# Optimization experiments

Measured on AMD Instinct MI355X. Metric: run time of the kernel, lower is better.

The kernel has to match this reference:

```python
import jax, jax.numpy as jnp
import numpy as np

N = 65536
E = 1048576
DIN = 64
DOUT = 64


def setup_inputs() -> dict:
    key = jax.random.key(0)
    ks = jax.random.split(key, 16)
    inp = {
        'feat': jax.random.normal(ks[0], (N, DIN), dtype=jnp.float32),
        'norm': jax.random.uniform(ks[1], (N, 1), dtype=jnp.float32),
        'src': jax.random.randint(ks[2], (E,), 0, N, dtype=jnp.int32),
        'dst': jax.random.randint(ks[3], (E,), 0, N, dtype=jnp.int32),
    }
    s = 0.05
    inp['W_self'] = jax.random.normal(ks[4], (DOUT, DIN)) * s
    inp['b_self'] = jnp.zeros((DOUT,), jnp.float32)
    inp['W_self_high'] = jax.random.normal(ks[5], (DOUT, DIN)) * s
    inp['b_self_high'] = jnp.zeros((DOUT,), jnp.float32)
    inp['W_neigh'] = jax.random.normal(ks[6], (DOUT, DIN)) * s
    inp['b_neigh'] = jnp.zeros((DOUT,), jnp.float32)
    inp['W_neigh_high'] = jax.random.normal(ks[7], (DOUT, DIN)) * s
    inp['b_neigh_high'] = jnp.zeros((DOUT,), jnp.float32)
    inp['W_id'] = jax.random.normal(ks[8], (DOUT, DIN)) * s
    inp['b_id'] = jnp.zeros((DOUT,), jnp.float32)
    inp['w_att_low'] = jax.random.normal(ks[9], (1, DOUT)) * s
    inp['w_att_high'] = jax.random.normal(ks[10], (1, DOUT)) * s
    inp['w_att_mlp'] = jax.random.normal(ks[11], (1, DOUT)) * s
    inp['W_att'] = jax.random.normal(ks[12], (3, 3)) * s
    return inp


def _linear(x, W, b):
    return x @ W.T + b


def _mean_agg(h, norm, src, dst, n_nodes):
    # copy_src('h','m') of (h * norm), then mean-reduce by dst node
    msg = (h * norm)[src]                                   # [E, D] gather
    summed = jax.ops.segment_sum(msg, dst, num_segments=n_nodes)
    deg = jax.ops.segment_sum(jnp.ones((dst.shape[0],), h.dtype), dst,
                              num_segments=n_nodes)
    return summed / jnp.maximum(deg, 1.0)[:, None]          # zero-in-degree -> 0


def reference(feat, norm, src, dst,
              W_self, b_self, W_self_high, b_self_high,
              W_neigh, b_neigh, W_neigh_high, b_neigh_high,
              W_id, b_id, w_att_low, w_att_high, w_att_mlp, W_att):
    n = feat.shape[0]
    # variant=True branch of acmgraphsage
    self_low = jax.nn.relu(_linear(feat, W_self, b_self))
    self_high = jax.nn.relu(_linear(feat, W_self_high, b_self_high))
    neigh_low = _mean_agg(jax.nn.relu(_linear(feat, W_neigh, b_neigh)),
                          norm, src, dst, n)
    neigh_high = _mean_agg(jax.nn.relu(_linear(feat, W_neigh_high, b_neigh_high)),
                           norm, src, dst, n)
    low = self_low + neigh_low
    high = self_high - neigh_high
    identity = jax.nn.relu(_linear(feat, W_id, b_id))
    # attention: sigmoid of per-branch scalar logits -> 3x3 mix -> softmax/T
    logits = jnp.concatenate([low @ w_att_low.T,
                              high @ w_att_high.T,
                              identity @ w_att_mlp.T], axis=1)   # [N, 3]
    att = jax.nn.softmax((jax.nn.sigmoid(logits) @ W_att.T) / 3.0, axis=1)
    rst = 3.0 * (att[:, 0:1] * low + att[:, 1:2] * high + att[:, 2:3] * identity)
    return rst
```

## Files before the change

### kernel.cpp

```cpp
#include <hip/hip_runtime.h>
#include <stdint.h>


#define NBLK 256
#define NBUC 1024
#define NPB  64
#define GCAP 2048
#define MTOT (NBUC * NBLK)

__device__ __forceinline__ void load_feat(const float* __restrict__ feat, size_t base,
                                          float* __restrict__ f) {
    const float4* fp = (const float4*)(feat + base);
#pragma unroll
    for (int i = 0; i < 16; ++i) {
        float4 v = fp[i];
        f[4 * i + 0] = v.x; f[4 * i + 1] = v.y;
        f[4 * i + 2] = v.z; f[4 * i + 3] = v.w;
    }
}

__device__ __forceinline__ uint32_t bf16_rne(float x) {
    uint32_t u = __float_as_uint(x);
    return (u + 0x7fffu + ((u >> 16) & 1u)) >> 16;
}

__global__ void __launch_bounds__(512)
k_transform(const float* __restrict__ feat, const float* __restrict__ norm,
            const float* __restrict__ Wn, const float* __restrict__ bn,
            const float* __restrict__ Wnh, const float* __restrict__ bnh,
            uint32_t* __restrict__ h_pk, int N)
{
    int t = threadIdx.x;
    int nsub = t & 63;
    int q = __builtin_amdgcn_readfirstlane(t >> 6);
    int n = blockIdx.x * 64 + nsub;
    if (n >= N) return;

    size_t base = (size_t)n << 6;
    float f[64];
    load_feat(feat, base, f);
    float nr = norm[n];

    uint32_t pk[8];
#pragma unroll
    for (int jj = 0; jj < 8; ++jj) {
        int j = q * 8 + jj;
        const float4* rL = (const float4*)(Wn  + ((size_t)j << 6));
        const float4* rH = (const float4*)(Wnh + ((size_t)j << 6));
        float sL = 0.f, sH = 0.f;
#pragma unroll
        for (int k4 = 0; k4 < 16; ++k4) {
            float4 wL = rL[k4];
            float4 wH = rH[k4];
            sL = fmaf(f[4*k4+0], wL.x, sL); sL = fmaf(f[4*k4+1], wL.y, sL);
            sL = fmaf(f[4*k4+2], wL.z, sL); sL = fmaf(f[4*k4+3], wL.w, sL);
            sH = fmaf(f[4*k4+0], wH.x, sH); sH = fmaf(f[4*k4+1], wH.y, sH);
            sH = fmaf(f[4*k4+2], wH.z, sH); sH = fmaf(f[4*k4+3], wH.w, sH);
        }
        float oL = fmaxf(sL + bn[j],  0.f) * nr;
        float oH = fmaxf(sH + bnh[j], 0.f) * nr;
        pk[jj] = bf16_rne(oL) | (bf16_rne(oH) << 16);
    }
    uint4* pp = (uint4*)(h_pk + base + q * 8);
    pp[0] = make_uint4(pk[0], pk[1], pk[2], pk[3]);
    pp[1] = make_uint4(pk[4], pk[5], pk[6], pk[7]);
}

__global__ void __launch_bounds__(512)
k_bin_hist(const int* __restrict__ dst, int* __restrict__ blk_cnt, int E)
{
    __shared__ int cnt[NBUC];
    int t = threadIdx.x;
    for (int i = t; i < NBUC; i += 512) cnt[i] = 0;
    __syncthreads();
    int epb = (E + NBLK - 1) / NBLK;
    int eb = blockIdx.x * epb;
    for (int i0 = t * 8; i0 < epb; i0 += 512 * 8) {
        int e = eb + i0;
        if (e + 8 <= E) {
            int4 d0 = *(const int4*)(dst + e);
            int4 d1 = *(const int4*)(dst + e + 4);
            atomicAdd(&cnt[((unsigned)d0.x) >> 6], 1);
            atomicAdd(&cnt[((unsigned)d0.y) >> 6], 1);
            atomicAdd(&cnt[((unsigned)d0.z) >> 6], 1);
            atomicAdd(&cnt[((unsigned)d0.w) >> 6], 1);
            atomicAdd(&cnt[((unsigned)d1.x) >> 6], 1);
            atomicAdd(&cnt[((unsigned)d1.y) >> 6], 1);
            atomicAdd(&cnt[((unsigned)d1.z) >> 6], 1);
            atomicAdd(&cnt[((unsigned)d1.w) >> 6], 1);
        } else {
            for (int j = 0; j < 8; ++j) {
                int ee = e + j;
                if (ee < E) atomicAdd(&cnt[((unsigned)dst[ee]) >> 6], 1);
            }
        }
    }
    __syncthreads();
    for (int i = t; i < NBUC; i += 512)
        blk_cnt[i * NBLK + blockIdx.x] = cnt[i];
}

__global__ void __launch_bounds__(256)
k_scan_part(const int* __restrict__ cnt_in, int* __restrict__ part)
{
    __shared__ int red[256];
    int t = threadIdx.x;
    const int4* A4 = (const int4*)cnt_in;
    int4 v = A4[blockIdx.x * 256 + t];
    int s = v.x + v.y + v.z + v.w;
    red[t] = s;
    __syncthreads();
    for (int off = 128; off > 0; off >>= 1) {
        if (t < off) red[t] += red[t + off];
        __syncthreads();
    }
    if (t == 0) part[blockIdx.x] = red[0];
}

__global__ void __launch_bounds__(256)
k_scan_top(const int* __restrict__ part, int* __restrict__ top)
{
    __shared__ int s[256];
    int t = threadIdx.x;
    int mine = part[t];
    s[t] = mine;
    __syncthreads();
    for (int off = 1; off < 256; off <<= 1) {
        int v = s[t];
        int a = (t >= off) ? s[t - off] : 0;
        __syncthreads();
        s[t] = v + a;
        __syncthreads();
    }
    top[t] = s[t] - mine;
}

__global__ void __launch_bounds__(256)
k_scan_down(const int* __restrict__ cnt_in, const int* __restrict__ top,
            int* __restrict__ off_out)
{
    __shared__ int s[256];
    int t = threadIdx.x;
    const int4* A4 = (const int4*)cnt_in;
    int4 v = A4[blockIdx.x * 256 + t];
    int sum = v.x + v.y + v.z + v.w;
    s[t] = sum;
    __syncthreads();
    for (int off = 1; off < 256; off <<= 1) {
        int vv = s[t];
        int a = (t >= off) ? s[t - off] : 0;
        __syncthreads();
        s[t] = vv + a;
        __syncthreads();
    }
    int run = top[blockIdx.x] + s[t] - sum;
    int4 o;
    o.x = run; run += v.x;
    o.y = run; run += v.y;
    o.z = run; run += v.z;
    o.w = run; run += v.w;
    ((int4*)off_out)[blockIdx.x * 256 + t] = o;
    if (blockIdx.x == 255 && t == 255) off_out[MTOT] = run;
}

__global__ void __launch_bounds__(512)
k_bin_scatter(const int* __restrict__ src, const int* __restrict__ dst,
              const int* __restrict__ blk_off, uint32_t* __restrict__ ebuf, int E)
{
    __shared__ int base_[NBUC];
    __shared__ int cnt[NBUC];
    int t = threadIdx.x;
    for (int i = t; i < NBUC; i += 512) {
        base_[i] = blk_off[i * NBLK + blockIdx.x];
        cnt[i] = 0;
    }
    __syncthreads();
    int epb = (E + NBLK - 1) / NBLK;
    int eb = blockIdx.x * epb;
    for (int i0 = t * 8; i0 < epb; i0 += 512 * 8) {
        int e = eb + i0;
        if (e + 8 <= E) {
            int4 d0 = *(const int4*)(dst + e);
            int4 d1 = *(const int4*)(dst + e + 4);
            int4 s0 = *(const int4*)(src + e);
            int4 s1 = *(const int4*)(src + e + 4);
            int da[8] = { d0.x, d0.y, d0.z, d0.w, d1.x, d1.y, d1.z, d1.w };
            int sa[8] = { s0.x, s0.y, s0.z, s0.w, s1.x, s1.y, s1.z, s1.w };
#pragma unroll
            for (int j = 0; j < 8; ++j) {
                int b = ((unsigned)da[j]) >> 6;
                int r = atomicAdd(&cnt[b], 1);
                ebuf[base_[b] + r] = ((uint32_t)(da[j] & 63) << 16) | (uint32_t)sa[j];
            }
        } else {
            for (int j = 0; j < 8; ++j) {
                int ee = e + j;
                if (ee < E) {
                    int d = dst[ee];
                    int b = ((unsigned)d) >> 6;
                    int r = atomicAdd(&cnt[b], 1);
                    ebuf[base_[b] + r] = ((uint32_t)(d & 63) << 16) | (uint32_t)src[ee];
                }
            }
        }
    }
}

__global__ void __launch_bounds__(512)
k_gf(const uint32_t* __restrict__ h_pk, const int* __restrict__ blk_off,
     const uint32_t* __restrict__ ebuf,
     const float* __restrict__ feat,
     const float* __restrict__ Ws, const float* __restrict__ bs,
     const float* __restrict__ Wsh, const float* __restrict__ bsh,
     const float* __restrict__ Wid, const float* __restrict__ bid,
     const float* __restrict__ wl, const float* __restrict__ wh,
     const float* __restrict__ wm, const float* __restrict__ Watt,
     float* __restrict__ out, int N)
{
    __shared__ unsigned short sorted[GCAP];
    __shared__ int s_cnt[NPB];
    __shared__ int s_off[NPB];
    __shared__ float s_mL[NPB][65];
    __shared__ float s_mH[NPB][65];
    __shared__ float red[3][8][64];

    int b = blockIdx.x;
    int t = threadIdx.x;
    int es = blk_off[b * NBLK];
    int ee = blk_off[(b + 1) * NBLK];
    int ne = ee - es;
    if (ne > GCAP) ne = GCAP;
    if (t < NPB) s_cnt[t] = 0;
    __syncthreads();

    int ed[4], er[4], esrc[4];
#pragma unroll
    for (int i = 0; i < 4; ++i) {
        int idx = i * 512 + t;
        ed[i] = -1;
        if (idx < ne) {
            uint32_t v = ebuf[es + idx];
            ed[i] = (int)(v >> 16);
            esrc[i] = (int)(v & 0xffffu);
            er[i] = atomicAdd(&s_cnt[ed[i]], 1);
        }
    }
    __syncthreads();
    if (t < 64) {
        int c = s_cnt[t];
        int sc = c;
        for (int o = 1; o < 64; o <<= 1) {
            int u = __shfl_up(sc, o, 64);
            if (t >= o) sc += u;
        }
        s_off[t] = sc - c;
    }
    __syncthreads();
#pragma unroll
    for (int i = 0; i < 4; ++i)
        if (ed[i] >= 0) sorted[s_off[ed[i]] + er[i]] = (unsigned short)esrc[i];
    __syncthreads();

    int w = t >> 6, lane = t & 63;
    for (int dd = 0; dd < 8; ++dd) {
        int d = w * 8 + dd;
        int cd = s_cnt[d];
        int od = s_off[d];
        float accL = 0.f, accH = 0.f;
        int i = 0;
        for (; i + 4 <= cd; i += 4) {
            int s0 = sorted[od + i + 0];
            int s1 = sorted[od + i + 1];
            int s2 = sorted[od + i + 2];
            int s3 = sorted[od + i + 3];
            uint32_t v0 = h_pk[((size_t)s0 << 6) + lane];
            uint32_t v1 = h_pk[((size_t)s1 << 6) + lane];
            uint32_t v2 = h_pk[((size_t)s2 << 6) + lane];
            uint32_t v3 = h_pk[((size_t)s3 << 6) + lane];
            accL += __uint_as_float(v0 << 16) + __uint_as_float(v1 << 16)
                  + __uint_as_float(v2 << 16) + __uint_as_float(v3 << 16);
            accH += __uint_as_float(v0 & 0xffff0000u) + __uint_as_float(v1 & 0xffff0000u)
                  + __uint_as_float(v2 & 0xffff0000u) + __uint_as_float(v3 & 0xffff0000u);
        }
        for (; i < cd; ++i) {
            int s0 = sorted[od + i];
            uint32_t v0 = h_pk[((size_t)s0 << 6) + lane];
            accL += __uint_as_float(v0 << 16);
            accH += __uint_as_float(v0 & 0xffff0000u);
        }
        float inv = 1.f / fmaxf((float)cd, 1.f);
        s_mL[d][lane] = accL * inv;
        s_mH[d][lane] = accH * inv;
    }
    __syncthreads();

    int nsub = t & 63;
    int q = __builtin_amdgcn_readfirstlane(t >> 6);
    int n = b * 64 + nsub;
    size_t base = (size_t)n << 6;

    float f[64];
    load_feat(feat, base, f);

    float aL[8], aH[8], aI[8];
    float dLp = 0.f, dHp = 0.f, dIp = 0.f;
#pragma unroll
    for (int jj = 0; jj < 8; ++jj) {
        int j = q * 8 + jj;
        const float4* rL = (const float4*)(Ws  + ((size_t)j << 6));
        const float4* rH = (const float4*)(Wsh + ((size_t)j << 6));
        const float4* rI = (const float4*)(Wid + ((size_t)j << 6));
        float sL = 0.f, sH = 0.f, sI = 0.f;
#pragma unroll
        for (int k4 = 0; k4 < 16; ++k4) {
            float4 wL = rL[k4];
            float4 wH = rH[k4];
            float4 wI = rI[k4];
            sL = fmaf(f[4*k4+0], wL.x, sL); sL = fmaf(f[4*k4+1], wL.y, sL);
            sL = fmaf(f[4*k4+2], wL.z, sL); sL = fmaf(f[4*k4+3], wL.w, sL);
            sH = fmaf(f[4*k4+0], wH.x, sH); sH = fmaf(f[4*k4+1], wH.y, sH);
            sH = fmaf(f[4*k4+2], wH.z, sH); sH = fmaf(f[4*k4+3], wH.w, sH);
            sI = fmaf(f[4*k4+0], wI.x, sI); sI = fmaf(f[4*k4+1], wI.y, sI);
            sI = fmaf(f[4*k4+2], wI.z, sI); sI = fmaf(f[4*k4+3], wI.w, sI);
        }
        float lowj  = fmaxf(sL + bs[j],  0.f) + s_mL[nsub][j];
        float highj = fmaxf(sH + bsh[j], 0.f) - s_mH[nsub][j];
        float idj   = fmaxf(sI + bid[j], 0.f);
        aL[jj] = lowj; aH[jj] = highj; aI[jj] = idj;
        dLp = fmaf(lowj,  wl[j], dLp);
        dHp = fmaf(highj, wh[j], dHp);
        dIp = fmaf(idj,   wm[j], dIp);
    }

    red[0][q][nsub] = dLp;
    red[1][q][nsub] = dHp;
    red[2][q][nsub] = dIp;
    __syncthreads();
    float dL = 0.f, dH = 0.f, dI = 0.f;
#pragma unroll
    for (int p = 0; p < 8; ++p) {
        dL += red[0][p][nsub];
        dH += red[1][p][nsub];
        dI += red[2][p][nsub];
    }

    float s0 = 1.f / (1.f + expf(-dL));
    float s1 = 1.f / (1.f + expf(-dH));
    float s2 = 1.f / (1.f + expf(-dI));
    const float third = (1.f / 3.f);
    float z0 = (Watt[0] * s0 + Watt[1] * s1 + Watt[2] * s2) * third;
    float z1 = (Watt[3] * s0 + Watt[4] * s1 + Watt[5] * s2) * third;
    float z2 = (Watt[6] * s0 + Watt[7] * s1 + Watt[8] * s2) * third;
    float m = fmaxf(z0, fmaxf(z1, z2));
    float e0 = expf(z0 - m), e1 = expf(z1 - m), e2 = expf(z2 - m);
    float r = 3.f / (e0 + e1 + e2);
    float a0 = e0 * r, a1 = e1 * r, a2 = e2 * r;

    float o[8];
#pragma unroll
    for (int jj = 0; jj < 8; ++jj)
        o[jj] = a0 * aL[jj] + a1 * aH[jj] + a2 * aI[jj];
    float* po = out + base + q * 8;
    *(float4*)(po + 0) = make_float4(o[0], o[1], o[2], o[3]);
    *(float4*)(po + 4) = make_float4(o[4], o[5], o[6], o[7]);
}

extern "C" void kernel_launch(void* const* d_in, const int* in_sizes, int n_in,
                              void* d_out, int out_size, void* d_ws, size_t ws_size,
                              hipStream_t stream) {
    const float* feat         = (const float*)d_in[0];
    const float* norm         = (const float*)d_in[1];
    const int*   src          = (const int*)d_in[2];
    const int*   dst          = (const int*)d_in[3];
    const float* W_self       = (const float*)d_in[4];
    const float* b_self       = (const float*)d_in[5];
    const float* W_self_high  = (const float*)d_in[6];
    const float* b_self_high  = (const float*)d_in[7];
    const float* W_neigh      = (const float*)d_in[8];
    const float* b_neigh      = (const float*)d_in[9];
    const float* W_neigh_high = (const float*)d_in[10];
    const float* b_neigh_high = (const float*)d_in[11];
    const float* W_id         = (const float*)d_in[12];
    const float* b_id         = (const float*)d_in[13];
    const float* w_att_low    = (const float*)d_in[14];
    const float* w_att_high   = (const float*)d_in[15];
    const float* w_att_mlp    = (const float*)d_in[16];
    const float* W_att        = (const float*)d_in[17];

    int N = in_sizes[0] / 64;
    int E = in_sizes[2];
    float* out = (float*)d_out;

    size_t N64 = (size_t)N * 64;

    uint32_t* h_pk    = (uint32_t*)d_ws;
    int*      blk_cnt = (int*)(h_pk + N64);
    int*      blk_off = blk_cnt + MTOT;
    int*      part    = blk_off + MTOT + 16;
    int*      top     = part + 256 + 16;
    uint32_t* ebuf    = (uint32_t*)(top + 256 + 16);

    dim3 gN64((N + 63) / 64);

    k_transform<<<gN64, dim3(512), 0, stream>>>(feat, norm, W_neigh, b_neigh,
                                                W_neigh_high, b_neigh_high,
                                                h_pk, N);
    k_bin_hist<<<dim3(NBLK), dim3(512), 0, stream>>>(dst, blk_cnt, E);
    k_scan_part<<<dim3(256), dim3(256), 0, stream>>>(blk_cnt, part);
    k_scan_top<<<dim3(1), dim3(256), 0, stream>>>(part, top);
    k_scan_down<<<dim3(256), dim3(256), 0, stream>>>(blk_cnt, top, blk_off);
    k_bin_scatter<<<dim3(NBLK), dim3(512), 0, stream>>>(src, dst, blk_off, ebuf, E);
    k_gf<<<dim3(NBUC), dim3(512), 0, stream>>>(h_pk, blk_off, ebuf, feat,
                                               W_self, b_self,
                                               W_self_high, b_self_high,
                                               W_id, b_id, w_att_low, w_att_high,
                                               w_att_mlp, W_att, out, N);
}
```

Measured before the change: 138.7 us.

## Fuse transform and histogram kernels, unroll gather by eight, pack mean in bf16

Merges the neighbour-transform kernel and the destination histogram kernel into one launch, where extra blocks do the histogram, so the two independent stages can overlap and one launch is saved. The gather loop gets an 8-wide unrolled path with pairwise summation, putting more independent loads in flight per warp. The per-node mean for the low and high branches is packed into one bf16x2 shared array, which halves that LDS footprint but adds another rounding of the aggregated values. The fused kernel now carries the 4 KB histogram shared array in every block, which may reduce occupancy for the transform blocks.

```diff
diff --git a/kernel.cpp b/kernel.cpp
--- a/kernel.cpp
+++ b/kernel.cpp
@@ -25,12 +25,48 @@
 }
 
 __global__ void __launch_bounds__(512)
-k_transform(const float* __restrict__ feat, const float* __restrict__ norm,
-            const float* __restrict__ Wn, const float* __restrict__ bn,
-            const float* __restrict__ Wnh, const float* __restrict__ bnh,
-            uint32_t* __restrict__ h_pk, int N)
-{
-    int t = threadIdx.x;
+k_tf_hist(const float* __restrict__ feat, const float* __restrict__ norm,
+          const float* __restrict__ Wn, const float* __restrict__ bn,
+          const float* __restrict__ Wnh, const float* __restrict__ bnh,
+          uint32_t* __restrict__ h_pk,
+          const int* __restrict__ dst, int* __restrict__ blk_cnt,
+          int N, int E, int nTf)
+{
+    __shared__ int cnt[NBUC];
+    int t = threadIdx.x;
+
+    if ((int)blockIdx.x >= nTf) {
+        int hb = blockIdx.x - nTf;
+        for (int i = t; i < NBUC; i += 512) cnt[i] = 0;
+        __syncthreads();
+        int epb = (E + NBLK - 1) / NBLK;
+        int eb = hb * epb;
+        for (int i0 = t * 8; i0 < epb; i0 += 512 * 8) {
+            int e = eb + i0;
+            if (e + 8 <= E) {
+                int4 d0 = *(const int4*)(dst + e);
+                int4 d1 = *(const int4*)(dst + e + 4);
+                atomicAdd(&cnt[((unsigned)d0.x) >> 6], 1);
+                atomicAdd(&cnt[((unsigned)d0.y) >> 6], 1);
+                atomicAdd(&cnt[((unsigned)d0.z) >> 6], 1);
+                atomicAdd(&cnt[((unsigned)d0.w) >> 6], 1);
+                atomicAdd(&cnt[((unsigned)d1.x) >> 6], 1);
+                atomicAdd(&cnt[((unsigned)d1.y) >> 6], 1);
+                atomicAdd(&cnt[((unsigned)d1.z) >> 6], 1);
+                atomicAdd(&cnt[((unsigned)d1.w) >> 6], 1);
+            } else {
+                for (int j = 0; j < 8; ++j) {
+                    int ee = e + j;
+                    if (ee < E) atomicAdd(&cnt[((unsigned)dst[ee]) >> 6], 1);
+                }
+            }
+        }
+        __syncthreads();
+        for (int i = t; i < NBUC; i += 512)
+            blk_cnt[i * NBLK + hb] = cnt[i];
+        return;
+    }
+
     int nsub = t & 63;
     int q = __builtin_amdgcn_readfirstlane(t >> 6);
     int n = blockIdx.x * 64 + nsub;
@@ -64,40 +100,6 @@
     uint4* pp = (uint4*)(h_pk + base + q * 8);
     pp[0] = make_uint4(pk[0], pk[1], pk[2], pk[3]);
     pp[1] = make_uint4(pk[4], pk[5], pk[6], pk[7]);
-}
-
-__global__ void __launch_bounds__(512)
-k_bin_hist(const int* __restrict__ dst, int* __restrict__ blk_cnt, int E)
-{
-    __shared__ int cnt[NBUC];
-    int t = threadIdx.x;
-    for (int i = t; i < NBUC; i += 512) cnt[i] = 0;
-    __syncthreads();
-    int epb = (E + NBLK - 1) / NBLK;
-    int eb = blockIdx.x * epb;
-    for (int i0 = t * 8; i0 < epb; i0 += 512 * 8) {
-        int e = eb + i0;
-        if (e + 8 <= E) {
-            int4 d0 = *(const int4*)(dst + e);
-            int4 d1 = *(const int4*)(dst + e + 4);
-            atomicAdd(&cnt[((unsigned)d0.x) >> 6], 1);
-            atomicAdd(&cnt[((unsigned)d0.y) >> 6], 1);
-            atomicAdd(&cnt[((unsigned)d0.z) >> 6], 1);
-            atomicAdd(&cnt[((unsigned)d0.w) >> 6], 1);
-            atomicAdd(&cnt[((unsigned)d1.x) >> 6], 1);
-            atomicAdd(&cnt[((unsigned)d1.y) >> 6], 1);
-            atomicAdd(&cnt[((unsigned)d1.z) >> 6], 1);
-            atomicAdd(&cnt[((unsigned)d1.w) >> 6], 1);
-        } else {
-            for (int j = 0; j < 8; ++j) {
-                int ee = e + j;
-                if (ee < E) atomicAdd(&cnt[((unsigned)dst[ee]) >> 6], 1);
-            }
-        }
-    }
-    __syncthreads();
-    for (int i = t; i < NBUC; i += 512)
-        blk_cnt[i * NBLK + blockIdx.x] = cnt[i];
 }
 
 __global__ void __launch_bounds__(256)
@@ -220,8 +222,7 @@
     __shared__ unsigned short sorted[GCAP];
     __shared__ int s_cnt[NPB];
     __shared__ int s_off[NPB];
-    __shared__ float s_mL[NPB][65];
-    __shared__ float s_mH[NPB][65];
+    __shared__ uint32_t s_m[NPB][65];
     __shared__ float red[3][8][64];
 
     int b = blockIdx.x;
@@ -268,6 +269,32 @@
         int od = s_off[d];
         float accL = 0.f, accH = 0.f;
         int i = 0;
+        for (; i + 8 <= cd; i += 8) {
+            int s0 = sorted[od + i + 0];
+            int s1 = sorted[od + i + 1];
+            int s2 = sorted[od + i + 2];
+            int s3 = sorted[od + i + 3];
+            int s4 = sorted[od + i + 4];
+            int s5 = sorted[od + i + 5];
+            int s6 = sorted[od + i + 6];
+            int s7 = sorted[od + i + 7];
+            uint32_t v0 = h_pk[((size_t)s0 << 6) + lane];
+            uint32_t v1 = h_pk[((size_t)s1 << 6) + lane];
+            uint32_t v2 = h_pk[((size_t)s2 << 6) + lane];
+            uint32_t v3 = h_pk[((size_t)s3 << 6) + lane];
+            uint32_t v4 = h_pk[((size_t)s4 << 6) + lane];
+            uint32_t v5 = h_pk[((size_t)s5 << 6) + lane];
+            uint32_t v6 = h_pk[((size_t)s6 << 6) + lane];
+            uint32_t v7 = h_pk[((size_t)s7 << 6) + lane];
+            accL += (__uint_as_float(v0 << 16) + __uint_as_float(v1 << 16))
+                  + (__uint_as_float(v2 << 16) + __uint_as_float(v3 << 16))
+                  + (__uint_as_float(v4 << 16) + __uint_as_float(v5 << 16))
+                  + (__uint_as_float(v6 << 16) + __uint_as_float(v7 << 16));
+            accH += (__uint_as_float(v0 & 0xffff0000u) + __uint_as_float(v1 & 0xffff0000u))
+                  + (__uint_as_float(v2 & 0xffff0000u) + __uint_as_float(v3 & 0xffff0000u))
+                  + (__uint_as_float(v4 & 0xffff0000u) + __uint_as_float(v5 & 0xffff0000u))
+                  + (__uint_as_float(v6 & 0xffff0000u) + __uint_as_float(v7 & 0xffff0000u));
+        }
         for (; i + 4 <= cd; i += 4) {
             int s0 = sorted[od + i + 0];
             int s1 = sorted[od + i + 1];
@@ -277,10 +304,10 @@
             uint32_t v1 = h_pk[((size_t)s1 << 6) + lane];
             uint32_t v2 = h_pk[((size_t)s2 << 6) + lane];
             uint32_t v3 = h_pk[((size_t)s3 << 6) + lane];
-            accL += __uint_as_float(v0 << 16) + __uint_as_float(v1 << 16)
-                  + __uint_as_float(v2 << 16) + __uint_as_float(v3 << 16);
-            accH += __uint_as_float(v0 & 0xffff0000u) + __uint_as_float(v1 & 0xffff0000u)
-                  + __uint_as_float(v2 & 0xffff0000u) + __uint_as_float(v3 & 0xffff0000u);
+            accL += (__uint_as_float(v0 << 16) + __uint_as_float(v1 << 16))
+                  + (__uint_as_float(v2 << 16) + __uint_as_float(v3 << 16));
+            accH += (__uint_as_float(v0 & 0xffff0000u) + __uint_as_float(v1 & 0xffff0000u))
+                  + (__uint_as_float(v2 & 0xffff0000u) + __uint_as_float(v3 & 0xffff0000u));
         }
         for (; i < cd; ++i) {
             int s0 = sorted[od + i];
@@ -289,8 +316,7 @@
             accH += __uint_as_float(v0 & 0xffff0000u);
         }
         float inv = 1.f / fmaxf((float)cd, 1.f);
-        s_mL[d][lane] = accL * inv;
-        s_mH[d][lane] = accH * inv;
+        s_m[d][lane] = bf16_rne(accL * inv) | (bf16_rne(accH * inv) << 16);
     }
     __syncthreads();
 
@@ -323,8 +349,9 @@
             sI = fmaf(f[4*k4+0], wI.x, sI); sI = fmaf(f[4*k4+1], wI.y, sI);
             sI = fmaf(f[4*k4+2], wI.z, sI); sI = fmaf(f[4*k4+3], wI.w, sI);
         }
-        float lowj  = fmaxf(sL + bs[j],  0.f) + s_mL[nsub][j];
-        float highj = fmaxf(sH + bsh[j], 0.f) - s_mH[nsub][j];
+        uint32_t mv = s_m[nsub][j];
+        float lowj  = fmaxf(sL + bs[j],  0.f) + __uint_as_float(mv << 16);
+        float highj = fmaxf(sH + bsh[j], 0.f) - __uint_as_float(mv & 0xffff0000u);
         float idj   = fmaxf(sI + bid[j], 0.f);
         aL[jj] = lowj; aH[jj] = highj; aI[jj] = idj;
         dLp = fmaf(lowj,  wl[j], dLp);
@@ -400,12 +427,11 @@
     int*      top     = part + 256 + 16;
     uint32_t* ebuf    = (uint32_t*)(top + 256 + 16);
 
-    dim3 gN64((N + 63) / 64);
-
-    k_transform<<<gN64, dim3(512), 0, stream>>>(feat, norm, W_neigh, b_neigh,
-                                                W_neigh_high, b_neigh_high,
-                                                h_pk, N);
-    k_bin_hist<<<dim3(NBLK), dim3(512), 0, stream>>>(dst, blk_cnt, E);
+    int nTf = (N + 63) / 64;
+
+    k_tf_hist<<<dim3(nTf + NBLK), dim3(512), 0, stream>>>(
+        feat, norm, W_neigh, b_neigh, W_neigh_high, b_neigh_high, h_pk,
+        dst, blk_cnt, N, E, nTf);
     k_scan_part<<<dim3(256), dim3(256), 0, stream>>>(blk_cnt, part);
     k_scan_top<<<dim3(1), dim3(256), 0, stream>>>(part, top);
     k_scan_down<<<dim3(256), dim3(256), 0, stream>>>(blk_cnt, top, blk_off);
```

After: 139.3 us. No clear change (+0.5%).
